# Performance work log

Hardware: AMD Instinct MI355X
Metric: run time of the kernel (lower is better)

Reference implementation:

```python
import jax, jax.numpy as jnp
import numpy as np

B, IN, V, H, OUT = 4096, 1024, 48, 512, 64

def setup_inputs() -> dict:
    key = jax.random.key(0)
    ks = jax.random.split(key, 6)
    s = 0.02
    x = jax.random.normal(ks[0], (B, IN), dtype=jnp.float32)
    # stacked per-vocab MLP params: hidden layers have bias, last layer bias=False
    W1 = jax.random.normal(ks[1], (V, IN, H), dtype=jnp.float32) * s
    b1 = jax.random.normal(ks[2], (V, H), dtype=jnp.float32) * s
    W2 = jax.random.normal(ks[3], (V, H, H), dtype=jnp.float32) * s
    b2 = jax.random.normal(ks[4], (V, H), dtype=jnp.float32) * s
    W3 = jax.random.normal(ks[5], (V, H, OUT), dtype=jnp.float32) * s
    return {"x": x, "W1": W1, "b1": b1, "W2": W2, "b2": b2, "W3": W3}

def reference(x, W1, b1, W2, b2, W3):
    # grouped GEMM over the vocab axis; equivalent to the per-MLP loop + cat
    h = jax.nn.relu(jnp.einsum('bi,vih->bvh', x, W1) + b1)      # [B, V, H]
    h = jax.nn.relu(jnp.einsum('bvh,vhk->bvk', h, W2) + b2)     # [B, V, H]
    o = jnp.einsum('bvk,vko->bvo', h, W3)                        # [B, V, OUT]
    # torch.cat([...], dim=-1) == reshape since outputs are in vocab order
    return o.reshape(x.shape[0], V * OUT)
```

## Files before the change

### kernel.cpp

```cpp
#include <hip/hip_runtime.h>

#define B_SZ   4096
#define IN_SZ  1024
#define V_SZ   48
#define H_SZ   512
#define OUT_SZ 64

typedef __attribute__((ext_vector_type(4))) float f32x4;
typedef __attribute__((ext_vector_type(8))) short bf16x8;
typedef __attribute__((ext_vector_type(4))) short short4v;
typedef __attribute__((ext_vector_type(4))) float float4v;

__device__ __forceinline__ short f2bf(float f){
    unsigned u = __builtin_bit_cast(unsigned, f);
    u += 0x7fffu + ((u >> 16) & 1u);
    return (short)(u >> 16);
}

__device__ __forceinline__ void gl2lds16(const void* g, void* l){
    __builtin_amdgcn_global_load_lds(
        (const __attribute__((address_space(1))) void*)g,
        (__attribute__((address_space(3))) void*)l, 16, 0, 0);
}

#define MFMA_B16(d, a, b) d = __builtin_amdgcn_mfma_f32_16x16x32_bf16(a, b, d, 0, 0, 0)

__global__ void k_convert_x(const float* __restrict__ x, short* __restrict__ xb){
    int i = blockIdx.x * 256 + threadIdx.x;
    float4v f = ((const float4v*)x)[i];
    short4v o = { f2bf(f.x), f2bf(f.y), f2bf(f.z), f2bf(f.w) };
    ((short4v*)xb)[i] = o;
}

__global__ __launch_bounds__(256) void k_transpose_cvt4(
    const float* __restrict__ in, short* __restrict__ out, int R, int C)
{
    __shared__ short t[64][68];
    int v  = blockIdx.z;
    int c0 = blockIdx.x * 64, r0 = blockIdx.y * 64;
    int tid = threadIdx.x;
    size_t base = (size_t)v * R * C;
    const float* inp = in + base + (size_t)r0 * C + c0;
    int g    = tid >> 4;
    int col4 = (tid & 15) * 4;
    #pragma unroll
    for (int p = 0; p < 4; ++p){
        int row = p*16 + g;
        float4v f = *(const float4v*)&inp[(size_t)row * C + col4];
        short4v s = { f2bf(f.x), f2bf(f.y), f2bf(f.z), f2bf(f.w) };
        *(short4v*)&t[row][col4] = s;
    }
    __syncthreads();
    short* outp = out + base + (size_t)c0 * R + r0;
    int r4 = (tid & 15) * 4;
    #pragma unroll
    for (int p = 0; p < 4; ++p){
        int c = p*16 + g;
        short4v s = { t[r4+0][c], t[r4+1][c], t[r4+2][c], t[r4+3][c] };
        *(short4v*)&outp[(size_t)c * R + r4] = s;
    }
}

#define G1_TILE (256*64)
#define G1_NT   (IN_SZ/64)

__global__ __launch_bounds__(512) void k_gemm1(
    const short* __restrict__ xb, const short* __restrict__ W1t,
    const float* __restrict__ b1, short* __restrict__ h1)
{
    __shared__ __align__(16) short As[2*G1_TILE];
    __shared__ __align__(16) short Bs[2*G1_TILE];
    const int tid  = threadIdx.x;
    const int lane = tid & 63, wave = tid >> 6;
    const int l15  = lane & 15, quad = lane >> 4;
    const int wm = wave >> 2, wn = wave & 3;
    const int M0 = blockIdx.x * 256;
    const int N0 = blockIdx.y * 256;
    const int v  = blockIdx.z;

    const short* apan = xb  + (size_t)M0 * IN_SZ;
    const short* bpan = W1t + ((size_t)v * H_SZ + N0) * IN_SZ;

    const int lr    = tid >> 3;
    const int toff  = lr * IN_SZ + (((tid & 7) ^ (lr & 7)) * 8);
    const int wbase = tid & ~63;

    auto stage = [&](const short* pan, short* lbase, int h, int j, int t){
        gl2lds16(pan + (size_t)(h*128 + j*64) * IN_SZ + t*64 + toff,
                 lbase + (h*1024 + j*512 + wbase) * 8);
    };
    auto stage_half = [&](const short* pan, short* lbase, int h, int t){
        stage(pan, lbase, h, 0, t);
        stage(pan, lbase, h, 1, t);
    };

    stage_half(apan, As, 0, 0); stage_half(apan, As, 1, 0);
    stage_half(bpan, Bs, 0, 0); stage_half(bpan, Bs, 1, 0);
    stage_half(apan, As + G1_TILE, 0, 1); stage_half(apan, As + G1_TILE, 1, 1);
    asm volatile("s_waitcnt vmcnt(4)" ::: "memory");
    __builtin_amdgcn_s_barrier();

    f32x4 acc[8][4];
    #pragma unroll
    for (int i = 0; i < 8; ++i)
        #pragma unroll
        for (int j = 0; j < 4; ++j) acc[i][j] = (f32x4){0.f,0.f,0.f,0.f};

    const int x7 = l15 & 7;
    const int abase = (wm*128 + l15) * 64;
    const int bbase = (wn*64  + l15) * 64;
    const int c_kk0 = ((quad)     ^ x7) * 8;
    const int c_kk1 = ((quad + 4) ^ x7) * 8;

    #pragma unroll 2
    for (int t = 0; t < G1_NT; ++t){
        short* Ac = As + (t & 1) * G1_TILE;
        short* Bc = Bs + (t & 1) * G1_TILE;
        short* Bn = Bs + ((t + 1) & 1) * G1_TILE;

        bf16x8 a0[8], a1[8];

        #pragma unroll
        for (int rf = 0; rf < 8; ++rf)
            a0[rf] = *(const bf16x8*)&Ac[abase + rf*1024 + c_kk0];
        bf16x8 b00 = *(const bf16x8*)&Bc[bbase + 0*1024 + c_kk0];
        bf16x8 b01 = *(const bf16x8*)&Bc[bbase + 1*1024 + c_kk0];
        if (t + 1 < G1_NT) stage_half(bpan, Bn, 0, t + 1);
        __builtin_amdgcn_s_barrier();
        asm volatile("s_waitcnt lgkmcnt(0)" ::: "memory");
        __builtin_amdgcn_s_setprio(1);
        #pragma unroll
        for (int rf = 0; rf < 8; ++rf){
            MFMA_B16(acc[rf][0], a0[rf], b00);
            MFMA_B16(acc[rf][1], a0[rf], b01);
        }
        __builtin_amdgcn_s_setprio(0);
        __builtin_amdgcn_s_barrier();

        #pragma unroll
        for (int rf = 0; rf < 8; ++rf)
            a1[rf] = *(const bf16x8*)&Ac[abase + rf*1024 + c_kk1];
        bf16x8 b02 = *(const bf16x8*)&Bc[bbase + 2*1024 + c_kk0];
        bf16x8 b03 = *(const bf16x8*)&Bc[bbase + 3*1024 + c_kk0];
        if (t + 1 < G1_NT) stage_half(bpan, Bn, 1, t + 1);
        __builtin_amdgcn_s_barrier();
        asm volatile("s_waitcnt lgkmcnt(0)" ::: "memory");
        __builtin_amdgcn_s_setprio(1);
        #pragma unroll
        for (int rf = 0; rf < 8; ++rf){
            MFMA_B16(acc[rf][2], a0[rf], b02);
            MFMA_B16(acc[rf][3], a0[rf], b03);
        }
        __builtin_amdgcn_s_setprio(0);
        __builtin_amdgcn_s_barrier();

        bf16x8 b10 = *(const bf16x8*)&Bc[bbase + 0*1024 + c_kk1];
        bf16x8 b11 = *(const bf16x8*)&Bc[bbase + 1*1024 + c_kk1];
        if (t + 2 < G1_NT) stage_half(apan, Ac, 0, t + 2);
        __builtin_amdgcn_s_barrier();
        asm volatile("s_waitcnt lgkmcnt(0)" ::: "memory");
        __builtin_amdgcn_s_setprio(1);
        #pragma unroll
        for (int rf = 0; rf < 8; ++rf){
            MFMA_B16(acc[rf][0], a1[rf], b10);
            MFMA_B16(acc[rf][1], a1[rf], b11);
        }
        __builtin_amdgcn_s_setprio(0);
        __builtin_amdgcn_s_barrier();

        bf16x8 b12 = *(const bf16x8*)&Bc[bbase + 2*1024 + c_kk1];
        bf16x8 b13 = *(const bf16x8*)&Bc[bbase + 3*1024 + c_kk1];
        if (t + 2 < G1_NT) stage_half(apan, Ac, 1, t + 2);
        __builtin_amdgcn_s_barrier();
        asm volatile("s_waitcnt lgkmcnt(0)" ::: "memory");
        __builtin_amdgcn_s_setprio(1);
        #pragma unroll
        for (int rf = 0; rf < 8; ++rf){
            MFMA_B16(acc[rf][2], a1[rf], b12);
            MFMA_B16(acc[rf][3], a1[rf], b13);
        }
        __builtin_amdgcn_s_setprio(0);
        if (t + 2 < G1_NT)      { asm volatile("s_waitcnt vmcnt(4)" ::: "memory"); }
        else if (t + 1 < G1_NT) { asm volatile("s_waitcnt vmcnt(0)" ::: "memory"); }
        __builtin_amdgcn_s_barrier();
    }

    const float* bv = b1 + (size_t)v * H_SZ;
    short* cv = h1 + (size_t)v * (B_SZ*H_SZ);
    #pragma unroll
    for (int cf = 0; cf < 4; ++cf){
        int col = N0 + wn*64 + cf*16 + l15;
        float bb = bv[col];
        #pragma unroll
        for (int rf = 0; rf < 8; ++rf){
            int rowb = M0 + wm*128 + rf*16 + quad*4;
            #pragma unroll
            for (int r = 0; r < 4; ++r){
                float val = acc[rf][cf][r] + bb;
                val = val > 0.f ? val : 0.f;
                cv[(size_t)(rowb + r) * H_SZ + col] = f2bf(val);
            }
        }
    }
}

__global__ __launch_bounds__(512) void k_gemm23(
    const short* __restrict__ h, const short* __restrict__ W2t,
    const float* __restrict__ b2, const short* __restrict__ W3t,
    float* __restrict__ out)
{
    __shared__ __align__(16) short As[64*64];
    __shared__ __align__(16) short Bs[512*64];
    const int tid  = threadIdx.x;
    const int lane = tid & 63, wave = tid >> 6;
    const int l15  = lane & 15, quad = lane >> 4;
    const int M0 = blockIdx.x * 64;
    const int v  = blockIdx.y;

    const short* hv  = h   + (size_t)v * (B_SZ*H_SZ) + (size_t)M0 * H_SZ;
    const short* w2v = W2t + (size_t)v * (H_SZ*H_SZ);
    const short* w3v = W3t + (size_t)v * (OUT_SZ*H_SZ);

    const int rowT = tid >> 3;
    const int wT   = (tid & 7) ^ (rowT & 7);
    const short* asrc  = hv  + (size_t)rowT * H_SZ + wT*8;
    const short* bsrc0 = w2v + (size_t)rowT * H_SZ + wT*8;
    short* adst  = &As[(size_t)(tid & ~63) * 8];
    short* bdst0 = &Bs[(size_t)(tid & ~63) * 8];

    f32x4 acc[4][4];
    #pragma unroll
    for (int i = 0; i < 4; ++i)
        #pragma unroll
        for (int j = 0; j < 4; ++j) acc[i][j] = (f32x4){0.f,0.f,0.f,0.f};

    for (int k0 = 0; k0 < H_SZ; k0 += 64){
        gl2lds16(asrc + k0, adst);
        #pragma unroll
        for (int j = 0; j < 8; ++j)
            gl2lds16(bsrc0 + (size_t)j*(64*H_SZ) + k0, bdst0 + (size_t)j*512*8);
        __syncthreads();
        #pragma unroll
        for (int kk = 0; kk < 2; ++kk){
            bf16x8 a[4], b[4];
            #pragma unroll
            for (int tm = 0; tm < 4; ++tm){
                int m = tm*16 + l15;
                int slot = m*8 + ((kk*4 + quad) ^ (m & 7));
                a[tm] = *(const bf16x8*)&As[slot*8];
            }
            #pragma unroll
            for (int tn = 0; tn < 4; ++tn){
                int n = wave*64 + tn*16 + l15;
                int slot = n*8 + ((kk*4 + quad) ^ (n & 7));
                b[tn] = *(const bf16x8*)&Bs[slot*8];
            }
            #pragma unroll
            for (int tm = 0; tm < 4; ++tm)
                #pragma unroll
                for (int tn = 0; tn < 4; ++tn)
                    acc[tm][tn] = __builtin_amdgcn_mfma_f32_16x16x32_bf16(
                        a[tm], b[tn], acc[tm][tn], 0, 0, 0);
        }
        __syncthreads();
    }

    const float* bv = b2 + (size_t)v * H_SZ;
    #pragma unroll
    for (int tn = 0; tn < 4; ++tn){
        int col = wave*64 + tn*16 + l15;
        float bb = bv[col];
        int u = col >> 3, c7 = col & 7;
        #pragma unroll
        for (int tm = 0; tm < 4; ++tm){
            int rowb = tm*16 + quad*4;
            #pragma unroll
            for (int r = 0; r < 4; ++r){
                int row = rowb + r;
                float val = acc[tm][tn][r] + bb;
                val = val > 0.f ? val : 0.f;
                Bs[row*512 + ((u ^ (row & 7))*8) + c7] = f2bf(val);
            }
        }
    }
    __syncthreads();

    if (wave < 4){
        f32x4 acc3[4];
        #pragma unroll
        for (int i = 0; i < 4; ++i) acc3[i] = (f32x4){0.f,0.f,0.f,0.f};
        const int n3 = wave*16 + l15;
        const short* b3p = &w3v[(size_t)n3 * H_SZ + quad*8];
        #pragma unroll
        for (int kk = 0; kk < 16; ++kk){
            bf16x8 bfrag = *(const bf16x8*)&b3p[kk*32];
            int u = kk*4 + quad;
            #pragma unroll
            for (int tm = 0; tm < 4; ++tm){
                int m = tm*16 + l15;
                bf16x8 afrag = *(const bf16x8*)&Bs[m*512 + ((u ^ (m & 7))*8)];
                acc3[tm] = __builtin_amdgcn_mfma_f32_16x16x32_bf16(
                    afrag, bfrag, acc3[tm], 0, 0, 0);
            }
        }
        const int col = v*OUT_SZ + wave*16 + l15;
        #pragma unroll
        for (int tm = 0; tm < 4; ++tm){
            int rowb = M0 + tm*16 + quad*4;
            #pragma unroll
            for (int r = 0; r < 4; ++r)
                out[(size_t)(rowb + r) * (V_SZ*OUT_SZ) + col] = acc3[tm][r];
        }
    }
}

extern "C" void kernel_launch(void* const* d_in, const int* in_sizes, int n_in,
                              void* d_out, int out_size, void* d_ws, size_t ws_size,
                              hipStream_t stream)
{
    (void)in_sizes; (void)n_in; (void)out_size; (void)ws_size;
    const float* x  = (const float*)d_in[0];
    const float* W1 = (const float*)d_in[1];
    const float* b1 = (const float*)d_in[2];
    const float* W2 = (const float*)d_in[3];
    const float* b2 = (const float*)d_in[4];
    const float* W3 = (const float*)d_in[5];
    float* out = (float*)d_out;

    char* ws = (char*)d_ws;
    short* xb  = (short*)ws;  ws += (size_t)B_SZ * IN_SZ * 2;
    short* W1t = (short*)ws;  ws += (size_t)V_SZ * H_SZ * IN_SZ * 2;
    short* W2t = (short*)ws;  ws += (size_t)V_SZ * H_SZ * H_SZ * 2;
    short* W3t = (short*)ws;  ws += (size_t)V_SZ * OUT_SZ * H_SZ * 2;
    short* h1  = (short*)ws;

    k_convert_x<<<dim3(B_SZ*IN_SZ/1024), dim3(256), 0, stream>>>(x, xb);
    k_transpose_cvt4<<<dim3(H_SZ/64,  IN_SZ/64, V_SZ), dim3(256), 0, stream>>>(W1, W1t, IN_SZ, H_SZ);
    k_transpose_cvt4<<<dim3(H_SZ/64,  H_SZ/64,  V_SZ), dim3(256), 0, stream>>>(W2, W2t, H_SZ, H_SZ);
    k_transpose_cvt4<<<dim3(OUT_SZ/64,H_SZ/64,  V_SZ), dim3(256), 0, stream>>>(W3, W3t, H_SZ, OUT_SZ);

    k_gemm1 <<<dim3(B_SZ/256, H_SZ/256, V_SZ), dim3(512), 0, stream>>>(xb, W1t, b1, h1);
    k_gemm23<<<dim3(B_SZ/64, V_SZ), dim3(512), 0, stream>>>(h1, W2t, b2, W3t, out);
}
```

Measured before the change: 655.8 us.

## Merge prepass kernels, raise gemm1 occupancy hint, spread layer-3 across all waves

Replaces the four conversion/transpose launches with a single prepass kernel that dispatches on block index, removing launch gaps and tail effects between them. Adds a min-blocks-per-CU hint of 2 to gemm1's launch bounds, which may force register limits or spills given its large LDS tiles. Splits the final layer-3 MFMA in gemm23 across all 8 waves (2x4 layout) instead of only 4, halving per-wave work and reducing idle waves.

Result: no change. 665.2 us (+1.4%).

```diff
diff --git a/kernel.cpp b/kernel.cpp
--- a/kernel.cpp
+++ b/kernel.cpp
@@ -25,20 +25,17 @@
 
 #define MFMA_B16(d, a, b) d = __builtin_amdgcn_mfma_f32_16x16x32_bf16(a, b, d, 0, 0, 0)
 
-__global__ void k_convert_x(const float* __restrict__ x, short* __restrict__ xb){
-    int i = blockIdx.x * 256 + threadIdx.x;
-    float4v f = ((const float4v*)x)[i];
-    short4v o = { f2bf(f.x), f2bf(f.y), f2bf(f.z), f2bf(f.w) };
-    ((short4v*)xb)[i] = o;
-}
-
-__global__ __launch_bounds__(256) void k_transpose_cvt4(
-    const float* __restrict__ in, short* __restrict__ out, int R, int C)
-{
-    __shared__ short t[64][68];
-    int v  = blockIdx.z;
-    int c0 = blockIdx.x * 64, r0 = blockIdx.y * 64;
-    int tid = threadIdx.x;
+#define PRE_CONV 4096
+#define PRE_W1   6144
+#define PRE_W2   3072
+#define PRE_W3   384
+#define PRE_NBLK (PRE_CONV + PRE_W1 + PRE_W2 + PRE_W3)
+
+__device__ __forceinline__ void transpose_cvt_body(
+    const float* __restrict__ in, short* __restrict__ out, int R, int C,
+    int bx, int by, int v, int tid, short (*t)[68])
+{
+    int c0 = bx * 64, r0 = by * 64;
     size_t base = (size_t)v * R * C;
     const float* inp = in + base + (size_t)r0 * C + c0;
     int g    = tid >> 4;
@@ -61,10 +58,36 @@
     }
 }
 
+__global__ __launch_bounds__(256) void k_prepass(
+    const float* __restrict__ x,  short* __restrict__ xb,
+    const float* __restrict__ W1, short* __restrict__ W1t,
+    const float* __restrict__ W2, short* __restrict__ W2t,
+    const float* __restrict__ W3, short* __restrict__ W3t)
+{
+    __shared__ short t[64][68];
+    const int bid = blockIdx.x;
+    const int tid = threadIdx.x;
+    if (bid < PRE_CONV){
+        int i = bid * 256 + tid;
+        float4v f = ((const float4v*)x)[i];
+        short4v o = { f2bf(f.x), f2bf(f.y), f2bf(f.z), f2bf(f.w) };
+        ((short4v*)xb)[i] = o;
+    } else if (bid < PRE_CONV + PRE_W1){
+        int l = bid - PRE_CONV;
+        transpose_cvt_body(W1, W1t, IN_SZ, H_SZ, l & 7, (l >> 3) & 15, l >> 7, tid, t);
+    } else if (bid < PRE_CONV + PRE_W1 + PRE_W2){
+        int l = bid - (PRE_CONV + PRE_W1);
+        transpose_cvt_body(W2, W2t, H_SZ, H_SZ, l & 7, (l >> 3) & 7, l >> 6, tid, t);
+    } else {
+        int l = bid - (PRE_CONV + PRE_W1 + PRE_W2);
+        transpose_cvt_body(W3, W3t, H_SZ, OUT_SZ, 0, l & 7, l >> 3, tid, t);
+    }
+}
+
 #define G1_TILE (256*64)
 #define G1_NT   (IN_SZ/64)
 
-__global__ __launch_bounds__(512) void k_gemm1(
+__global__ __launch_bounds__(512, 2) void k_gemm1(
     const short* __restrict__ xb, const short* __restrict__ W1t,
     const float* __restrict__ b1, short* __restrict__ h1)
 {
@@ -285,31 +308,33 @@
     }
     __syncthreads();
 
-    if (wave < 4){
-        f32x4 acc3[4];
-        #pragma unroll
-        for (int i = 0; i < 4; ++i) acc3[i] = (f32x4){0.f,0.f,0.f,0.f};
-        const int n3 = wave*16 + l15;
+    {
+        const int wm3 = wave >> 2;
+        const int wn3 = wave & 3;
+        f32x4 acc3[2];
+        #pragma unroll
+        for (int i = 0; i < 2; ++i) acc3[i] = (f32x4){0.f,0.f,0.f,0.f};
+        const int n3 = wn3*16 + l15;
         const short* b3p = &w3v[(size_t)n3 * H_SZ + quad*8];
         #pragma unroll
         for (int kk = 0; kk < 16; ++kk){
             bf16x8 bfrag = *(const bf16x8*)&b3p[kk*32];
             int u = kk*4 + quad;
             #pragma unroll
-            for (int tm = 0; tm < 4; ++tm){
-                int m = tm*16 + l15;
+            for (int mf = 0; mf < 2; ++mf){
+                int m = wm3*32 + mf*16 + l15;
                 bf16x8 afrag = *(const bf16x8*)&Bs[m*512 + ((u ^ (m & 7))*8)];
-                acc3[tm] = __builtin_amdgcn_mfma_f32_16x16x32_bf16(
-                    afrag, bfrag, acc3[tm], 0, 0, 0);
-            }
-        }
-        const int col = v*OUT_SZ + wave*16 + l15;
-        #pragma unroll
-        for (int tm = 0; tm < 4; ++tm){
-            int rowb = M0 + tm*16 + quad*4;
+                acc3[mf] = __builtin_amdgcn_mfma_f32_16x16x32_bf16(
+                    afrag, bfrag, acc3[mf], 0, 0, 0);
+            }
+        }
+        const int col = v*OUT_SZ + wn3*16 + l15;
+        #pragma unroll
+        for (int mf = 0; mf < 2; ++mf){
+            int rowb = M0 + wm3*32 + mf*16 + quad*4;
             #pragma unroll
             for (int r = 0; r < 4; ++r)
-                out[(size_t)(rowb + r) * (V_SZ*OUT_SZ) + col] = acc3[tm][r];
+                out[(size_t)(rowb + r) * (V_SZ*OUT_SZ) + col] = acc3[mf][r];
         }
     }
 }
@@ -334,10 +359,7 @@
     short* W3t = (short*)ws;  ws += (size_t)V_SZ * OUT_SZ * H_SZ * 2;
     short* h1  = (short*)ws;
 
-    k_convert_x<<<dim3(B_SZ*IN_SZ/1024), dim3(256), 0, stream>>>(x, xb);
-    k_transpose_cvt4<<<dim3(H_SZ/64,  IN_SZ/64, V_SZ), dim3(256), 0, stream>>>(W1, W1t, IN_SZ, H_SZ);
-    k_transpose_cvt4<<<dim3(H_SZ/64,  H_SZ/64,  V_SZ), dim3(256), 0, stream>>>(W2, W2t, H_SZ, H_SZ);
-    k_transpose_cvt4<<<dim3(OUT_SZ/64,H_SZ/64,  V_SZ), dim3(256), 0, stream>>>(W3, W3t, H_SZ, OUT_SZ);
+    k_prepass<<<dim3(PRE_NBLK), dim3(256), 0, stream>>>(x, xb, W1, W1t, W2, W2t, W3, W3t);
 
     k_gemm1 <<<dim3(B_SZ/256, H_SZ/256, V_SZ), dim3(512), 0, stream>>>(xb, W1t, b1, h1);
     k_gemm23<<<dim3(B_SZ/64, V_SZ), dim3(512), 0, stream>>>(h1, W2t, b2, W3t, out);
```
